# Performance work log

Measured on AMD Instinct MI355X. Metric: run time of the kernel, lower is better.

The kernel has to match this reference:

```python
import jax, jax.numpy as jnp
import numpy as np

N_EVENTS = 16
N_SAMPLES = 2 ** 15          # 32768
STEP = 256                   # window_size // 2
LONG_WINDOW = 4096
LONG_COEFFS = LONG_WINDOW // 2 + 1   # 2049
LONG_STEP = LONG_WINDOW // 2         # 2048
LONG_FRAMES = N_SAMPLES // LONG_STEP # 16
N_FRAMES = N_SAMPLES // STEP         # 128
B = 8                                 # audio batch
BE = B * N_EVENTS                     # event batch = 128


def setup_inputs() -> dict:
    key = jax.random.key(0)
    k1, k2, k3, k4 = jax.random.split(key, 4)
    env = jax.random.uniform(k1, (BE, LONG_WINDOW, LONG_FRAMES), jnp.float32)
    tf = jax.random.normal(k2, (BE, LONG_COEFFS * 2, LONG_FRAMES), jnp.float32)
    noise = jax.random.uniform(k3, (BE, LONG_WINDOW, LONG_FRAMES), jnp.float32)
    indices = jax.random.randint(k4, (B, N_EVENTS), 0, N_FRAMES, dtype=jnp.int32)
    return {"env": env, "tf": tf, "noise": noise, "indices": indices}


def _event_render(env, tf, noise):
    # env, noise: (BE, LONG_WINDOW, LONG_FRAMES); tf: (BE, 2*LONG_COEFFS, LONG_FRAMES)
    batch = env.shape[0]
    energy = env * (noise * 2.0 - 1.0)  # uniform_(-1, 1) noise scaled by amp

    # magnitude = norm over interleaved (real, imag) pairs, per torch view semantics
    pairs = tf.reshape(batch, LONG_COEFFS, 2, LONG_FRAMES)
    mag = jnp.sqrt(jnp.sum(pairs * pairs, axis=2))  # (batch, C, F)
    mx = jnp.max(mag.reshape(batch, -1), axis=-1, keepdims=True)
    mag = (mag.reshape(batch, -1) / (mx + 1e-8)).reshape(batch, LONG_COEFFS, LONG_FRAMES)
    imag = tf[:, LONG_COEFFS:, :]
    phase = jnp.arctan2(imag, mag) * np.pi  # torch.angle(complex(mag, imag)) * pi
    tfc = mag * jnp.exp(1j * phase)         # complex transfer fn (batch, C, F)

    # sequential per-frame recurrence: state feeds through rfft/irfft filtering
    e_t = jnp.transpose(energy, (2, 0, 1))  # (F, batch, W)
    t_t = jnp.transpose(tfc, (2, 0, 1))     # (F, batch, C)

    def step(prev, inp):
        e, t = inp
        local = prev + e
        spec = jnp.fft.rfft(local, axis=-1, norm='ortho') * t
        frame = jnp.fft.irfft(spec, n=LONG_WINDOW, axis=-1, norm='ortho')
        return frame, frame

    init = jnp.zeros((batch, LONG_WINDOW), energy.dtype)
    _, frames = jax.lax.scan(step, init, (e_t, t_t))   # (F, batch, W)
    frames = jnp.transpose(frames, (1, 0, 2))          # (batch, F, W)

    # overlap-add with hop = LONG_STEP = W/2: split frames into halves and add
    halves = frames.reshape(batch, LONG_FRAMES, 2, LONG_STEP)
    out = jnp.zeros((batch, LONG_FRAMES + 1, LONG_STEP), frames.dtype)
    out = out.at[:, :LONG_FRAMES].add(halves[:, :, 0])
    out = out.at[:, 1:].add(halves[:, :, 1])
    return out.reshape(batch, -1)[:, :N_SAMPLES]       # (BE, N_SAMPLES)


def _segment_render(atoms, indices):
    # atoms: (BE, N_SAMPLES) -> (B, N_EVENTS, N_SAMPLES); scatter-add at time offsets
    x = atoms.reshape(B, N_EVENTS, N_SAMPLES)
    times = indices * STEP                                      # (B, E)
    pos = times[:, :, None] + jnp.arange(N_SAMPLES)[None, None, :]  # (B, E, S)
    out = jnp.zeros((B, 2 * N_SAMPLES), x.dtype)
    bidx = jnp.arange(B)[:, None, None]
    out = out.at[bidx, pos].add(x)
    return out[:, None, :N_SAMPLES]                             # (B, 1, N_SAMPLES)


def reference(env, tf, noise, indices):
    atoms = _event_render(env, tf, noise)
    return _segment_render(atoms, indices)
```

## Files before the change

kernel.cpp:

```cpp
#include <hip/hip_runtime.h>
#include <math.h>

#define TWO_PI 6.283185307179586f

#define OFF_ET   0ull
#define OFF_E    8388608ull
#define OFF_MAXP 16781312ull
#define OFF_Z    16782336ull

__device__ __forceinline__ int swz(int n) { return n ^ ((n >> 5) & 31); }

__device__ __forceinline__ int permf(int k) {
    return ((k & 1) << 10) | (((k >> 1) & 3) << 8) | (((k >> 3) & 3) << 6)
         | (((k >> 5) & 3) << 4) | (((k >> 7) & 3) << 2) | ((k >> 9) & 3);
}

__device__ __forceinline__ void r4f_core(float* cr, float* ci, int p0, int p1, int p2, int p3,
                                         float c1, float s1, float c2, float s2, float c3, float s3) {
    float ar = cr[p0], ai = ci[p0];
    float br = cr[p1], bi = ci[p1];
    float crr = cr[p2], cri = ci[p2];
    float drr = cr[p3], dri = ci[p3];
    float u0r = ar + crr, u0i = ai + cri;
    float u1r = ar - crr, u1i = ai - cri;
    float u2r = br + drr, u2i = bi + dri;
    float u3r = br - drr, u3i = bi - dri;
    cr[p0] = u0r + u2r; ci[p0] = u0i + u2i;
    float z1r = u1r + u3i, z1i = u1i - u3r;
    cr[p1] = z1r * c1 + z1i * s1; ci[p1] = z1i * c1 - z1r * s1;
    float z2r = u0r - u2r, z2i = u0i - u2i;
    cr[p2] = z2r * c2 + z2i * s2; ci[p2] = z2i * c2 - z2r * s2;
    float z3r = u1r - u3i, z3i = u1i + u3r;
    cr[p3] = z3r * c3 + z3i * s3; ci[p3] = z3i * c3 - z3r * s3;
}

__device__ __forceinline__ void r4i_core(float* cr, float* ci, int p0, int p1, int p2, int p3,
                                         float c1, float s1, float c2, float s2, float c3, float s3) {
    float z0r = cr[p0], z0i = ci[p0];
    float z1r = cr[p1], z1i = ci[p1];
    float z2r = cr[p2], z2i = ci[p2];
    float z3r = cr[p3], z3i = ci[p3];
    float t1r = z1r * c1 - z1i * s1, t1i = z1i * c1 + z1r * s1;
    float t2r = z2r * c2 - z2i * s2, t2i = z2i * c2 + z2r * s2;
    float t3r = z3r * c3 - z3i * s3, t3i = z3i * c3 + z3r * s3;
    float u0r = z0r + t2r, u0i = z0i + t2i;
    float u1r = z0r - t2r, u1i = z0i - t2i;
    float u2r = t1r + t3r, u2i = t1i + t3i;
    float u3r = t1r - t3r, u3i = t1i - t3i;
    cr[p0] = u0r + u2r; ci[p0] = u0i + u2i;
    cr[p1] = u1r - u3i; ci[p1] = u1i + u3r;
    cr[p2] = u0r - u2r; ci[p2] = u0i - u2i;
    cr[p3] = u1r + u3i; ci[p3] = u1i - u3r;
}

#define STAGE4X(CORE, JEXPR, H, ANGEXPR)                                       \
    {                                                                          \
        _Pragma("unroll")                                                      \
        for (int half_ = 0; half_ < 2; ++half_) {                              \
            int b_ = tid + half_ * 1024;                                       \
            int i_ = b_ & 511;                                                 \
            float* cr_ = B + (b_ >> 9) * 4096;                                 \
            int j_ = (JEXPR);                                                  \
            int p0 = swz(j_), p1 = swz(j_ + (H)), p2 = swz(j_ + 2 * (H)),      \
                p3 = swz(j_ + 3 * (H));                                        \
            float s1, c1; __sincosf((ANGEXPR), &s1, &c1);                      \
            float c2 = c1 * c1 - s1 * s1, s2 = 2.f * c1 * s1;                  \
            float c3 = c1 * c2 - s1 * s2, s3 = s1 * c2 + c1 * s2;              \
            CORE(cr_, cr_ + 2048, p0, p1, p2, p3, c1, s1, c2, s2, c3, s3);     \
        }                                                                      \
    }                                                                          \
    __syncthreads();

__global__ __launch_bounds__(1024, 8) void k_fwd(const float* __restrict__ env,
                                                 const float* __restrict__ noise,
                                                 const float* __restrict__ tf,
                                                 float* __restrict__ ws) {
    __shared__ float B[16384];
    int tid = threadIdx.x;
    int id = blockIdx.x;
    int xcd = id & 7, slot = id >> 3;
    int be = xcd * 16 + (slot >> 2);
    int fg = slot & 3;
    const float4* env4 = (const float4*)env;
    const float4* noi4 = (const float4*)noise;
    size_t base = (size_t)be * 16384 + fg;

    float4 ev[4], nv[4];
#pragma unroll
    for (int it = 0; it < 4; ++it) {
        int n = it * 1024 + tid;
        ev[it] = env4[base + (size_t)n * 4];
        nv[it] = noi4[base + (size_t)n * 4];
    }
#pragma unroll
    for (int it = 0; it < 4; ++it) {
        int n = it * 1024 + tid;
        float4 e = ev[it], z = nv[it];
        float v0 = e.x * (z.x * 2.0f - 1.0f);
        float v1 = e.y * (z.y * 2.0f - 1.0f);
        float v2 = e.z * (z.z * 2.0f - 1.0f);
        float v3 = e.w * (z.w * 2.0f - 1.0f);
        int m = swz(n >> 1) + (n & 1) * 2048;
        B[m] = v0; B[4096 + m] = v1; B[8192 + m] = v2; B[12288 + m] = v3;
    }
    __syncthreads();
    {
        int i = tid;
        int sj = swz(i), sjb = swz(i + 1024);
        float s, c; __sincosf((float)i * (TWO_PI / 2048.0f), &s, &c);
#pragma unroll
        for (int j4 = 0; j4 < 4; ++j4) {
            float* cr = B + j4 * 4096;
            float* ci = cr + 2048;
            float ar = cr[sj], ai = ci[sj], br = cr[sjb], bi = ci[sjb];
            float dr = ar - br, di = ai - bi;
            cr[sj] = ar + br; ci[sj] = ai + bi;
            cr[sjb] = dr * c + di * s; ci[sjb] = di * c - dr * s;
        }
    }
    __syncthreads();
    STAGE4X(r4f_core, (i_ >> 8) * 1024 + (i_ & 255), 256, (float)(i_ & 255) * (TWO_PI / 1024.0f));
    STAGE4X(r4f_core, (i_ >> 6) * 256 + (i_ & 63), 64, (float)(i_ & 63) * (TWO_PI / 256.0f));
    STAGE4X(r4f_core, (i_ & 31) * 64 + (i_ >> 5), 16, (float)(i_ >> 5) * (TWO_PI / 64.0f));
    STAGE4X(r4f_core, (i_ & 127) * 16 + (i_ >> 7), 4, (float)(i_ >> 7) * (TWO_PI / 16.0f));
    STAGE4X(r4f_core, i_ * 4, 1, 0.0f);
    float2* Ebase = (float2*)(ws + OFF_E) + (size_t)(be * 16 + fg * 4) * 2049;
    for (int k = tid; k <= 1024; k += 1024) {
        int pk = swz(permf(k));
        int pm = swz(permf((2048 - k) & 2047));
        float s4, c4; __sincosf((float)k * (TWO_PI / 4096.0f), &s4, &c4);
#pragma unroll
        for (int j4 = 0; j4 < 4; ++j4) {
            float* cr = B + j4 * 4096;
            float* ci = cr + 2048;
            float zkr = cr[pk], zki = ci[pk], zmr = cr[pm], zmi = ci[pm];
            float xer = 0.5f * (zkr + zmr), xei = 0.5f * (zki - zmi);
            float xor_ = 0.5f * (zki + zmi), xoi = 0.5f * (zmr - zkr);
            float wr = xor_ * c4 + xoi * s4;
            float wi = xoi * c4 - xor_ * s4;
            float2* Eg = Ebase + (size_t)j4 * 2049;
            Eg[k] = make_float2(xer + wr, xei + wi);
            Eg[2048 - k] = make_float2(xer - wr, wi - xei);
        }
    }
    __syncthreads();
    const float4* ab4 = (const float4*)(tf + (size_t)be * 65568);
    int b0 = fg * 513;
    int nb = (fg == 3) ? 510 : 513;
    float mx = 0.f;
    for (int u = tid; u < nb * 4; u += 1024) {
        int g = u >> 2, e = u & 3;
        int bin = b0 + g;
        float4 A = ab4[bin * 8 + e];
        float4 Bv = ab4[bin * 8 + e + 4];
        mx = fmaxf(mx, fmaxf(fmaxf(A.x * A.x + Bv.x * Bv.x, A.y * A.y + Bv.y * Bv.y),
                             fmaxf(A.z * A.z + Bv.z * Bv.z, A.w * A.w + Bv.w * Bv.w)));
    }
    B[tid] = mx;
    __syncthreads();
    for (int s = 512; s > 0; s >>= 1) {
        if (tid < s) B[tid] = fmaxf(B[tid], B[tid + s]);
        __syncthreads();
    }
    if (tid == 0) ws[OFF_MAXP + be * 4 + fg] = B[0];
}

__global__ __launch_bounds__(256) void k_recur(const float* __restrict__ tf,
                                               float* __restrict__ ws) {
    __shared__ float sm2lo[256 * 17], simlo[256 * 17];
    __shared__ float sm2hi[256 * 17], simhi[256 * 17];
    int tid = threadIdx.x;
    int be = blockIdx.y;
    int k0 = blockIdx.x << 8;
    int hi0 = 1793 - k0;
    const float* tfb = tf + (size_t)be * 65568;
    const float4* ab4 = (const float4*)tfb;
    const float4* im4 = (const float4*)(tfb + 32784);

    for (int u = tid; u < 2048; u += 256) {
        int half = u >> 10, v = u & 1023;
        int g = v >> 2, e = v & 3;
        int bin = half ? (hi0 + g) : (k0 + g);
        float4 A = ab4[bin * 8 + e];
        float4 Bv = ab4[bin * 8 + e + 4];
        float4 I = im4[bin * 4 + e];
        int o = g * 17 + e * 4;
        float* sm = half ? sm2hi : sm2lo;
        float* si = half ? simhi : simlo;
        sm[o + 0] = A.x * A.x + Bv.x * Bv.x;
        sm[o + 1] = A.y * A.y + Bv.y * Bv.y;
        sm[o + 2] = A.z * A.z + Bv.z * Bv.z;
        sm[o + 3] = A.w * A.w + Bv.w * Bv.w;
        si[o + 0] = I.x; si[o + 1] = I.y; si[o + 2] = I.z; si[o + 3] = I.w;
    }
    __syncthreads();

    int k = k0 + tid;
    int m = 2048 - k;
    int rhi = 255 - tid;
    const float* mp = ws + OFF_MAXP + be * 4;
    float m2x = fmaxf(fmaxf(mp[0], mp[1]), fmaxf(mp[2], mp[3]));
    float rden = 1.0f / (sqrtf(m2x) + 1e-8f);
    const float2* Eb = (const float2*)(ws + OFF_E) + (size_t)be * 16 * 2049;
    float2* Zb = (float2*)(ws + OFF_Z) + (size_t)be * 16 * 2048;
    float2 evlo[16], evhi[16];
#pragma unroll
    for (int f = 0; f < 16; ++f) {
        evlo[f] = Eb[(size_t)f * 2049 + k];
        evhi[f] = Eb[(size_t)f * 2049 + m];
    }
    float ym = (k == 0) ? 0.0f : 1.0f;
    float s4, c4; __sincosf((float)k * (TWO_PI / 4096.0f), &s4, &c4);
    const float SCL = 1.0f / 2048.0f;
    float srl = 0.f, sil = 0.f, srh = 0.f, sih = 0.f;
#pragma unroll
    for (int f = 0; f < 16; ++f) {
        float mh = sqrtf(sm2lo[tid * 17 + f]) * rden;
        float ph = atan2f(simlo[tid * 17 + f], mh) * 3.14159265358979f;
        float sp, cp; __sincosf(ph, &sp, &cp);
        float Tr = mh * cp, Ti = mh * sp;
        sil *= ym;
        srl += evlo[f].x; sil += evlo[f].y;
        float nr = srl * Tr - sil * Ti;
        sil = srl * Ti + sil * Tr; srl = nr;
        float mh2 = sqrtf(sm2hi[rhi * 17 + f]) * rden;
        float ph2 = atan2f(simhi[rhi * 17 + f], mh2) * 3.14159265358979f;
        float sp2, cp2; __sincosf(ph2, &sp2, &cp2);
        float Tr2 = mh2 * cp2, Ti2 = mh2 * sp2;
        sih *= ym;
        srh += evhi[f].x; sih += evhi[f].y;
        float nr2 = srh * Tr2 - sih * Ti2;
        sih = srh * Ti2 + sih * Tr2; srh = nr2;
        float2* Zf = Zb + (size_t)f * 2048;
        if (k == 0) {
            float y0 = srl * SCL, yn = srh * SCL;
            Zf[0] = make_float2(0.5f * (y0 + yn), 0.5f * (y0 - yn));
        } else {
            float ykr = srl * SCL, yki = sil * SCL;
            float ymr = srh * SCL, ymi = sih * SCL;
            float er = 0.5f * (ykr + ymr), ei = 0.5f * (yki - ymi);
            float dr = ykr - ymr, di = yki + ymi;
            float orr = 0.5f * (dr * c4 - di * s4);
            float oi = 0.5f * (dr * s4 + di * c4);
            Zf[k] = make_float2(er - oi, ei + orr);
            Zf[m] = make_float2(er + oi, orr - ei);
        }
    }
    if (k0 == 0 && tid == 0) {
        float sr = 0.f, si = 0.f;
#pragma unroll
        for (int f = 0; f < 16; ++f) {
            float a = tfb[1024 * 32 + f];
            float b = tfb[1024 * 32 + 16 + f];
            float im = tfb[32784 + 1024 * 16 + f];
            float mh = sqrtf(a * a + b * b) * rden;
            float ph = atan2f(im, mh) * 3.14159265358979f;
            float sp, cp; __sincosf(ph, &sp, &cp);
            float Tr = mh * cp, Ti = mh * sp;
            float2 e = Eb[(size_t)f * 2049 + 1024];
            sr += e.x; si += e.y;
            float nr = sr * Tr - si * Ti;
            si = sr * Ti + si * Tr; sr = nr;
            Zb[(size_t)f * 2048 + 1024] = make_float2(sr * SCL, -si * SCL);
        }
    }
}

__global__ __launch_bounds__(1024, 8) void k_fft_inv(float* __restrict__ ws) {
    __shared__ float B[16384];
    int tid = threadIdx.x;
    int be = blockIdx.x >> 2, fg = blockIdx.x & 3;
    const float2* Zbase = (const float2*)(ws + OFF_Z) + (size_t)(be * 16 + fg * 4) * 2048;
    float4 v[4];
#pragma unroll
    for (int j4 = 0; j4 < 4; ++j4)
        v[j4] = ((const float4*)(Zbase + (size_t)j4 * 2048))[tid];
#pragma unroll
    for (int j4 = 0; j4 < 4; ++j4) {
        float* cr = B + j4 * 4096;
        float* ci = cr + 2048;
        int n0 = tid * 2;
        int p0 = swz(permf(n0)), p1 = swz(permf(n0 + 1));
        cr[p0] = v[j4].x; ci[p0] = v[j4].y;
        cr[p1] = v[j4].z; ci[p1] = v[j4].w;
    }
    __syncthreads();
    STAGE4X(r4i_core, i_ * 4, 1, 0.0f);
    STAGE4X(r4i_core, (i_ & 127) * 16 + (i_ >> 7), 4, (float)(i_ >> 7) * (TWO_PI / 16.0f));
    STAGE4X(r4i_core, (i_ & 31) * 64 + (i_ >> 5), 16, (float)(i_ >> 5) * (TWO_PI / 64.0f));
    STAGE4X(r4i_core, (i_ >> 6) * 256 + (i_ & 63), 64, (float)(i_ & 63) * (TWO_PI / 256.0f));
    STAGE4X(r4i_core, (i_ >> 8) * 1024 + (i_ & 255), 256, (float)(i_ & 255) * (TWO_PI / 1024.0f));
    {
        int i = tid;
        int sj = swz(i), sjb = swz(i + 1024);
        float s, c; __sincosf((float)i * (TWO_PI / 2048.0f), &s, &c);
#pragma unroll
        for (int j4 = 0; j4 < 4; ++j4) {
            float* cr = B + j4 * 4096;
            float* ci = cr + 2048;
            float br = cr[sjb], bi = ci[sjb];
            float tr = br * c - bi * s, ti2 = br * s + bi * c;
            float ar = cr[sj], ai = ci[sj];
            cr[sj] = ar + tr;  ci[sj] = ai + ti2;
            cr[sjb] = ar - tr; ci[sjb] = ai - ti2;
        }
    }
    __syncthreads();
    float2* Fbase = (float2*)(ws + OFF_ET) + (size_t)(be * 16 + fg * 4) * 2048;
#pragma unroll
    for (int j4 = 0; j4 < 4; ++j4) {
        float* cr = B + j4 * 4096;
        float* ci = cr + 2048;
        float2* Fg = Fbase + (size_t)j4 * 2048;
#pragma unroll
        for (int it = 0; it < 2; ++it) {
            int m = tid + it * 1024;
            Fg[m] = make_float2(cr[swz(m)], ci[swz(m)]);
        }
    }
}

__global__ __launch_bounds__(256) void k_segment(const float* __restrict__ ws,
                                                 const int* __restrict__ indices,
                                                 float* __restrict__ out) {
    __shared__ int ste[16];
    int tid = threadIdx.x;
    int b = blockIdx.y;
    if (tid < 16) ste[tid] = indices[b * 16 + tid] * 256;
    __syncthreads();
    int g = blockIdx.x * 256 + tid;
    int t = g << 2;
    const float* F = ws + OFF_ET;
    float4 acc = make_float4(0.f, 0.f, 0.f, 0.f);
#pragma unroll
    for (int e = 0; e < 16; ++e) {
        int te = ste[e];
        if (t >= te) {
            int d = t - te;
            int j = d >> 11, r = d & 2047;
            size_t base = (size_t)(b * 16 + e) * 65536;
            float4 v = *(const float4*)(F + base + j * 4096 + r);
            acc.x += v.x; acc.y += v.y; acc.z += v.z; acc.w += v.w;
            if (j >= 1) {
                float4 w = *(const float4*)(F + base + (j - 1) * 4096 + 2048 + r);
                acc.x += w.x; acc.y += w.y; acc.z += w.z; acc.w += w.w;
            }
        }
    }
    ((float4*)out)[(size_t)b * 8192 + g] = acc;
}

extern "C" void kernel_launch(void* const* d_in, const int* in_sizes, int n_in,
                              void* d_out, int out_size, void* d_ws, size_t ws_size,
                              hipStream_t stream) {
    const float* env = (const float*)d_in[0];
    const float* tf = (const float*)d_in[1];
    const float* noise = (const float*)d_in[2];
    const int* indices = (const int*)d_in[3];
    float* ws = (float*)d_ws;
    float* out = (float*)d_out;

    k_fwd<<<dim3(512), dim3(1024), 0, stream>>>(env, noise, tf, ws);
    k_recur<<<dim3(4, 128), dim3(256), 0, stream>>>(tf, ws);
    k_fft_inv<<<dim3(512), dim3(1024), 0, stream>>>(ws);
    k_segment<<<dim3(32, 8), dim3(256), 0, stream>>>(ws, indices, out);
}
```

Before: 82.25 us.

## Store FFT shared-memory buffers as interleaved float2 with new swizzle and stage indexing

Switches the shared-memory FFT workspace in the forward and inverse kernels from split real/imag float arrays to interleaved float2. Each complex element now moves with one 64-bit LDS access instead of two 32-bit ones, and the XOR swizzle is narrowed to match the 8-byte element width. The thread-to-butterfly mapping of the middle radix-4 stages is also changed so consecutive threads touch consecutive elements. The aim is fewer LDS instructions and fewer bank conflicts, at the risk of a different conflict pattern for 64-bit accesses.

```diff
diff --git a/kernel.cpp b/kernel.cpp
--- a/kernel.cpp
+++ b/kernel.cpp
@@ -8,49 +8,43 @@
 #define OFF_MAXP 16781312ull
 #define OFF_Z    16782336ull
 
-__device__ __forceinline__ int swz(int n) { return n ^ ((n >> 5) & 31); }
+__device__ __forceinline__ int sw2(int n) { return n ^ ((n >> 4) & 15); }
 
 __device__ __forceinline__ int permf(int k) {
     return ((k & 1) << 10) | (((k >> 1) & 3) << 8) | (((k >> 3) & 3) << 6)
          | (((k >> 5) & 3) << 4) | (((k >> 7) & 3) << 2) | ((k >> 9) & 3);
 }
 
-__device__ __forceinline__ void r4f_core(float* cr, float* ci, int p0, int p1, int p2, int p3,
+__device__ __forceinline__ void r4f_core(float2* b, int p0, int p1, int p2, int p3,
                                          float c1, float s1, float c2, float s2, float c3, float s3) {
-    float ar = cr[p0], ai = ci[p0];
-    float br = cr[p1], bi = ci[p1];
-    float crr = cr[p2], cri = ci[p2];
-    float drr = cr[p3], dri = ci[p3];
-    float u0r = ar + crr, u0i = ai + cri;
-    float u1r = ar - crr, u1i = ai - cri;
-    float u2r = br + drr, u2i = bi + dri;
-    float u3r = br - drr, u3i = bi - dri;
-    cr[p0] = u0r + u2r; ci[p0] = u0i + u2i;
+    float2 A = b[p0], Bv = b[p1], C = b[p2], D = b[p3];
+    float u0r = A.x + C.x, u0i = A.y + C.y;
+    float u1r = A.x - C.x, u1i = A.y - C.y;
+    float u2r = Bv.x + D.x, u2i = Bv.y + D.y;
+    float u3r = Bv.x - D.x, u3i = Bv.y - D.y;
+    b[p0] = make_float2(u0r + u2r, u0i + u2i);
     float z1r = u1r + u3i, z1i = u1i - u3r;
-    cr[p1] = z1r * c1 + z1i * s1; ci[p1] = z1i * c1 - z1r * s1;
+    b[p1] = make_float2(z1r * c1 + z1i * s1, z1i * c1 - z1r * s1);
     float z2r = u0r - u2r, z2i = u0i - u2i;
-    cr[p2] = z2r * c2 + z2i * s2; ci[p2] = z2i * c2 - z2r * s2;
+    b[p2] = make_float2(z2r * c2 + z2i * s2, z2i * c2 - z2r * s2);
     float z3r = u1r - u3i, z3i = u1i + u3r;
-    cr[p3] = z3r * c3 + z3i * s3; ci[p3] = z3i * c3 - z3r * s3;
-}
-
-__device__ __forceinline__ void r4i_core(float* cr, float* ci, int p0, int p1, int p2, int p3,
+    b[p3] = make_float2(z3r * c3 + z3i * s3, z3i * c3 - z3r * s3);
+}
+
+__device__ __forceinline__ void r4i_core(float2* b, int p0, int p1, int p2, int p3,
                                          float c1, float s1, float c2, float s2, float c3, float s3) {
-    float z0r = cr[p0], z0i = ci[p0];
-    float z1r = cr[p1], z1i = ci[p1];
-    float z2r = cr[p2], z2i = ci[p2];
-    float z3r = cr[p3], z3i = ci[p3];
-    float t1r = z1r * c1 - z1i * s1, t1i = z1i * c1 + z1r * s1;
-    float t2r = z2r * c2 - z2i * s2, t2i = z2i * c2 + z2r * s2;
-    float t3r = z3r * c3 - z3i * s3, t3i = z3i * c3 + z3r * s3;
-    float u0r = z0r + t2r, u0i = z0i + t2i;
-    float u1r = z0r - t2r, u1i = z0i - t2i;
+    float2 z0 = b[p0], z1 = b[p1], z2 = b[p2], z3 = b[p3];
+    float t1r = z1.x * c1 - z1.y * s1, t1i = z1.y * c1 + z1.x * s1;
+    float t2r = z2.x * c2 - z2.y * s2, t2i = z2.y * c2 + z2.x * s2;
+    float t3r = z3.x * c3 - z3.y * s3, t3i = z3.y * c3 + z3.x * s3;
+    float u0r = z0.x + t2r, u0i = z0.y + t2i;
+    float u1r = z0.x - t2r, u1i = z0.y - t2i;
     float u2r = t1r + t3r, u2i = t1i + t3i;
     float u3r = t1r - t3r, u3i = t1i - t3i;
-    cr[p0] = u0r + u2r; ci[p0] = u0i + u2i;
-    cr[p1] = u1r - u3i; ci[p1] = u1i + u3r;
-    cr[p2] = u0r - u2r; ci[p2] = u0i - u2i;
-    cr[p3] = u1r + u3i; ci[p3] = u1i - u3r;
+    b[p0] = make_float2(u0r + u2r, u0i + u2i);
+    b[p1] = make_float2(u1r - u3i, u1i + u3r);
+    b[p2] = make_float2(u0r - u2r, u0i - u2i);
+    b[p3] = make_float2(u1r + u3i, u1i - u3r);
 }
 
 #define STAGE4X(CORE, JEXPR, H, ANGEXPR)                                       \
@@ -59,14 +53,14 @@
         for (int half_ = 0; half_ < 2; ++half_) {                              \
             int b_ = tid + half_ * 1024;                                       \
             int i_ = b_ & 511;                                                 \
-            float* cr_ = B + (b_ >> 9) * 4096;                                 \
+            float2* bb_ = B2 + (b_ >> 9) * 2048;                               \
             int j_ = (JEXPR);                                                  \
-            int p0 = swz(j_), p1 = swz(j_ + (H)), p2 = swz(j_ + 2 * (H)),      \
-                p3 = swz(j_ + 3 * (H));                                        \
+            int p0 = sw2(j_), p1 = sw2(j_ + (H)), p2 = sw2(j_ + 2 * (H)),      \
+                p3 = sw2(j_ + 3 * (H));                                        \
             float s1, c1; __sincosf((ANGEXPR), &s1, &c1);                      \
             float c2 = c1 * c1 - s1 * s1, s2 = 2.f * c1 * s1;                  \
             float c3 = c1 * c2 - s1 * s2, s3 = s1 * c2 + c1 * s2;              \
-            CORE(cr_, cr_ + 2048, p0, p1, p2, p3, c1, s1, c2, s2, c3, s3);     \
+            CORE(bb_, p0, p1, p2, p3, c1, s1, c2, s2, c3, s3);                 \
         }                                                                      \
     }                                                                          \
     __syncthreads();
@@ -75,7 +69,7 @@
                                                  const float* __restrict__ noise,
                                                  const float* __restrict__ tf,
                                                  float* __restrict__ ws) {
-    __shared__ float B[16384];
+    __shared__ float2 B2[8192];
     int tid = threadIdx.x;
     int id = blockIdx.x;
     int xcd = id & 7, slot = id >> 3;
@@ -85,57 +79,50 @@
     const float4* noi4 = (const float4*)noise;
     size_t base = (size_t)be * 16384 + fg;
 
-    float4 ev[4], nv[4];
-#pragma unroll
-    for (int it = 0; it < 4; ++it) {
-        int n = it * 1024 + tid;
-        ev[it] = env4[base + (size_t)n * 4];
-        nv[it] = noi4[base + (size_t)n * 4];
-    }
-#pragma unroll
-    for (int it = 0; it < 4; ++it) {
-        int n = it * 1024 + tid;
-        float4 e = ev[it], z = nv[it];
-        float v0 = e.x * (z.x * 2.0f - 1.0f);
-        float v1 = e.y * (z.y * 2.0f - 1.0f);
-        float v2 = e.z * (z.z * 2.0f - 1.0f);
-        float v3 = e.w * (z.w * 2.0f - 1.0f);
-        int m = swz(n >> 1) + (n & 1) * 2048;
-        B[m] = v0; B[4096 + m] = v1; B[8192 + m] = v2; B[12288 + m] = v3;
+#pragma unroll
+    for (int it = 0; it < 2; ++it) {
+        int c = tid + it * 1024;
+        float4 ea = env4[base + (size_t)(2 * c) * 4];
+        float4 eb = env4[base + (size_t)(2 * c + 1) * 4];
+        float4 za = noi4[base + (size_t)(2 * c) * 4];
+        float4 zb = noi4[base + (size_t)(2 * c + 1) * 4];
+        int m = sw2(c);
+        B2[m]        = make_float2(ea.x * (za.x * 2.f - 1.f), eb.x * (zb.x * 2.f - 1.f));
+        B2[2048 + m] = make_float2(ea.y * (za.y * 2.f - 1.f), eb.y * (zb.y * 2.f - 1.f));
+        B2[4096 + m] = make_float2(ea.z * (za.z * 2.f - 1.f), eb.z * (zb.z * 2.f - 1.f));
+        B2[6144 + m] = make_float2(ea.w * (za.w * 2.f - 1.f), eb.w * (zb.w * 2.f - 1.f));
     }
     __syncthreads();
     {
         int i = tid;
-        int sj = swz(i), sjb = swz(i + 1024);
+        int sj = sw2(i), sjb = sw2(i + 1024);
         float s, c; __sincosf((float)i * (TWO_PI / 2048.0f), &s, &c);
 #pragma unroll
         for (int j4 = 0; j4 < 4; ++j4) {
-            float* cr = B + j4 * 4096;
-            float* ci = cr + 2048;
-            float ar = cr[sj], ai = ci[sj], br = cr[sjb], bi = ci[sjb];
-            float dr = ar - br, di = ai - bi;
-            cr[sj] = ar + br; ci[sj] = ai + bi;
-            cr[sjb] = dr * c + di * s; ci[sjb] = di * c - dr * s;
+            float2* bb = B2 + j4 * 2048;
+            float2 a = bb[sj], b = bb[sjb];
+            float dr = a.x - b.x, di = a.y - b.y;
+            bb[sj] = make_float2(a.x + b.x, a.y + b.y);
+            bb[sjb] = make_float2(dr * c + di * s, di * c - dr * s);
         }
     }
     __syncthreads();
     STAGE4X(r4f_core, (i_ >> 8) * 1024 + (i_ & 255), 256, (float)(i_ & 255) * (TWO_PI / 1024.0f));
     STAGE4X(r4f_core, (i_ >> 6) * 256 + (i_ & 63), 64, (float)(i_ & 63) * (TWO_PI / 256.0f));
-    STAGE4X(r4f_core, (i_ & 31) * 64 + (i_ >> 5), 16, (float)(i_ >> 5) * (TWO_PI / 64.0f));
-    STAGE4X(r4f_core, (i_ & 127) * 16 + (i_ >> 7), 4, (float)(i_ >> 7) * (TWO_PI / 16.0f));
+    STAGE4X(r4f_core, (i_ >> 4) * 64 + (i_ & 15), 16, (float)(i_ & 15) * (TWO_PI / 64.0f));
+    STAGE4X(r4f_core, (i_ >> 2) * 16 + (i_ & 3), 4, (float)(i_ & 3) * (TWO_PI / 16.0f));
     STAGE4X(r4f_core, i_ * 4, 1, 0.0f);
     float2* Ebase = (float2*)(ws + OFF_E) + (size_t)(be * 16 + fg * 4) * 2049;
     for (int k = tid; k <= 1024; k += 1024) {
-        int pk = swz(permf(k));
-        int pm = swz(permf((2048 - k) & 2047));
+        int pk = sw2(permf(k));
+        int pm = sw2(permf((2048 - k) & 2047));
         float s4, c4; __sincosf((float)k * (TWO_PI / 4096.0f), &s4, &c4);
 #pragma unroll
         for (int j4 = 0; j4 < 4; ++j4) {
-            float* cr = B + j4 * 4096;
-            float* ci = cr + 2048;
-            float zkr = cr[pk], zki = ci[pk], zmr = cr[pm], zmi = ci[pm];
-            float xer = 0.5f * (zkr + zmr), xei = 0.5f * (zki - zmi);
-            float xor_ = 0.5f * (zki + zmi), xoi = 0.5f * (zmr - zkr);
+            float2* bb = B2 + j4 * 2048;
+            float2 zk = bb[pk], zm = bb[pm];
+            float xer = 0.5f * (zk.x + zm.x), xei = 0.5f * (zk.y - zm.y);
+            float xor_ = 0.5f * (zk.y + zm.y), xoi = 0.5f * (zm.x - zk.x);
             float wr = xor_ * c4 + xoi * s4;
             float wi = xoi * c4 - xor_ * s4;
             float2* Eg = Ebase + (size_t)j4 * 2049;
@@ -144,6 +131,7 @@
         }
     }
     __syncthreads();
+    float* Bf = (float*)B2;
     const float4* ab4 = (const float4*)(tf + (size_t)be * 65568);
     int b0 = fg * 513;
     int nb = (fg == 3) ? 510 : 513;
@@ -156,13 +144,13 @@
         mx = fmaxf(mx, fmaxf(fmaxf(A.x * A.x + Bv.x * Bv.x, A.y * A.y + Bv.y * Bv.y),
                              fmaxf(A.z * A.z + Bv.z * Bv.z, A.w * A.w + Bv.w * Bv.w)));
     }
-    B[tid] = mx;
+    Bf[tid] = mx;
     __syncthreads();
     for (int s = 512; s > 0; s >>= 1) {
-        if (tid < s) B[tid] = fmaxf(B[tid], B[tid + s]);
+        if (tid < s) Bf[tid] = fmaxf(Bf[tid], Bf[tid + s]);
         __syncthreads();
     }
-    if (tid == 0) ws[OFF_MAXP + be * 4 + fg] = B[0];
+    if (tid == 0) ws[OFF_MAXP + be * 4 + fg] = Bf[0];
 }
 
 __global__ __launch_bounds__(256) void k_recur(const float* __restrict__ tf,
@@ -267,7 +255,7 @@
 }
 
 __global__ __launch_bounds__(1024, 8) void k_fft_inv(float* __restrict__ ws) {
-    __shared__ float B[16384];
+    __shared__ float2 B2[8192];
     int tid = threadIdx.x;
     int be = blockIdx.x >> 2, fg = blockIdx.x & 3;
     const float2* Zbase = (const float2*)(ws + OFF_Z) + (size_t)(be * 16 + fg * 4) * 2048;
@@ -275,47 +263,46 @@
 #pragma unroll
     for (int j4 = 0; j4 < 4; ++j4)
         v[j4] = ((const float4*)(Zbase + (size_t)j4 * 2048))[tid];
-#pragma unroll
-    for (int j4 = 0; j4 < 4; ++j4) {
-        float* cr = B + j4 * 4096;
-        float* ci = cr + 2048;
+    {
         int n0 = tid * 2;
-        int p0 = swz(permf(n0)), p1 = swz(permf(n0 + 1));
-        cr[p0] = v[j4].x; ci[p0] = v[j4].y;
-        cr[p1] = v[j4].z; ci[p1] = v[j4].w;
+        int p0 = sw2(permf(n0)), p1 = sw2(permf(n0 + 1));
+#pragma unroll
+        for (int j4 = 0; j4 < 4; ++j4) {
+            float2* bb = B2 + j4 * 2048;
+            bb[p0] = make_float2(v[j4].x, v[j4].y);
+            bb[p1] = make_float2(v[j4].z, v[j4].w);
+        }
     }
     __syncthreads();
     STAGE4X(r4i_core, i_ * 4, 1, 0.0f);
-    STAGE4X(r4i_core, (i_ & 127) * 16 + (i_ >> 7), 4, (float)(i_ >> 7) * (TWO_PI / 16.0f));
-    STAGE4X(r4i_core, (i_ & 31) * 64 + (i_ >> 5), 16, (float)(i_ >> 5) * (TWO_PI / 64.0f));
+    STAGE4X(r4i_core, (i_ >> 2) * 16 + (i_ & 3), 4, (float)(i_ & 3) * (TWO_PI / 16.0f));
+    STAGE4X(r4i_core, (i_ >> 4) * 64 + (i_ & 15), 16, (float)(i_ & 15) * (TWO_PI / 64.0f));
     STAGE4X(r4i_core, (i_ >> 6) * 256 + (i_ & 63), 64, (float)(i_ & 63) * (TWO_PI / 256.0f));
     STAGE4X(r4i_core, (i_ >> 8) * 1024 + (i_ & 255), 256, (float)(i_ & 255) * (TWO_PI / 1024.0f));
     {
         int i = tid;
-        int sj = swz(i), sjb = swz(i + 1024);
+        int sj = sw2(i), sjb = sw2(i + 1024);
         float s, c; __sincosf((float)i * (TWO_PI / 2048.0f), &s, &c);
 #pragma unroll
         for (int j4 = 0; j4 < 4; ++j4) {
-            float* cr = B + j4 * 4096;
-            float* ci = cr + 2048;
-            float br = cr[sjb], bi = ci[sjb];
-            float tr = br * c - bi * s, ti2 = br * s + bi * c;
-            float ar = cr[sj], ai = ci[sj];
-            cr[sj] = ar + tr;  ci[sj] = ai + ti2;
-            cr[sjb] = ar - tr; ci[sjb] = ai - ti2;
+            float2* bb = B2 + j4 * 2048;
+            float2 b = bb[sjb];
+            float tr = b.x * c - b.y * s, ti2 = b.x * s + b.y * c;
+            float2 a = bb[sj];
+            bb[sj] = make_float2(a.x + tr, a.y + ti2);
+            bb[sjb] = make_float2(a.x - tr, a.y - ti2);
         }
     }
     __syncthreads();
     float2* Fbase = (float2*)(ws + OFF_ET) + (size_t)(be * 16 + fg * 4) * 2048;
 #pragma unroll
     for (int j4 = 0; j4 < 4; ++j4) {
-        float* cr = B + j4 * 4096;
-        float* ci = cr + 2048;
+        float2* bb = B2 + j4 * 2048;
         float2* Fg = Fbase + (size_t)j4 * 2048;
 #pragma unroll
         for (int it = 0; it < 2; ++it) {
             int m = tid + it * 1024;
-            Fg[m] = make_float2(cr[swz(m)], ci[swz(m)]);
+            Fg[m] = bb[sw2(m)];
         }
     }
 }
```

New measurement: 88.72 us. 1.08x slower.
